# Optimization experiments

Hardware: AMD Instinct MI355X
Metric: run time of the kernel (lower is better)

The kernel has to match this reference:

```python
import jax, jax.numpy as jnp
import numpy as np

# Matcher thresholds from detectron2 RPN defaults
IOU_LO, IOU_HI = 0.3, 0.7            # anchor_matcher
OBJ_LO, OBJ_HI = 0.1, 0.3            # objectness_anchor_matcher (lower thresholds)
EPS = 1e-12


def _pairwise_iou(gt, anc):
    # gt: [G,4], anc: [A,4] (x1,y1,x2,y2) -> [G,A]
    area_g = (gt[:, 2] - gt[:, 0]) * (gt[:, 3] - gt[:, 1])
    area_a = (anc[:, 2] - anc[:, 0]) * (anc[:, 3] - anc[:, 1])
    lt = jnp.maximum(gt[:, None, :2], anc[None, :, :2])
    rb = jnp.minimum(gt[:, None, 2:], anc[None, :, 2:])
    wh = jnp.clip(rb - lt, 0.0)
    inter = wh[..., 0] * wh[..., 1]
    union = area_g[:, None] + area_a[None, :] - inter
    return jnp.where(inter > 0, inter / union, 0.0)


def _match(iou, lo, hi):
    # detectron2 Matcher with labels [0,-1,1] and allow_low_quality_matches=True
    vals = iou.max(axis=0)                      # [A]
    idxs = jnp.argmax(iou, axis=0)              # [A]
    labels = jnp.where(vals >= hi, 1, jnp.where(vals >= lo, -1, 0)).astype(jnp.int32)
    highest_per_gt = iou.max(axis=1)            # [G]
    low_quality = (iou == highest_per_gt[:, None]).any(axis=0)  # [A]
    labels = jnp.where(low_quality, 1, labels)
    return idxs, labels


def _get_deltas_linear(anc, tgt):
    # Box2BoxTransformLinear(normalize_by_size=True).get_deltas
    cx = 0.5 * (anc[:, 0] + anc[:, 2])
    cy = 0.5 * (anc[:, 1] + anc[:, 3])
    w = anc[:, 2] - anc[:, 0]
    h = anc[:, 3] - anc[:, 1]
    # order (l, t, r, b)
    deltas = jnp.stack([cx - tgt[:, 0], cy - tgt[:, 1], tgt[:, 2] - cx, tgt[:, 3] - cy], axis=-1)
    return deltas / jnp.stack([w, h, w, h], axis=-1)


def _label_one_image(gt_i, anchors):
    iou = _pairwise_iou(gt_i, anchors)                     # [G,A]
    m_idx, gt_labels = _match(iou, IOU_LO, IOU_HI)
    o_idx, obj_labels = _match(iou, OBJ_LO, OBJ_HI)
    matched_gt_boxes = gt_i[m_idx]                         # [A,4]
    # deltas reordered [:, [0,2,1,3]] -> (left, right, top, bottom)
    d = _get_deltas_linear(anchors, gt_i[o_idx])[:, jnp.array([0, 2, 1, 3])]
    in_box = (d >= 0).all(axis=-1)
    d = jnp.where(in_box[:, None], d, 0.0)
    lr, tb = d[:, 0:2], d[:, 2:4]
    prod = (lr.min(-1) / (lr.max(-1) + EPS)) * (tb.min(-1) / (tb.max(-1) + EPS))
    centerness = jnp.where(prod > 0, jnp.sqrt(jnp.where(prod > 0, prod, 1.0)), 0.0)
    centerness = jnp.where(obj_labels == 0, 0.0, centerness)
    return gt_labels, matched_gt_boxes, obj_labels, centerness


def setup_inputs() -> dict:
    key = jax.random.key(0)
    k1, k2, k3, k4 = jax.random.split(key, 4)
    A, B, G = 200000, 8, 32
    img_wh = jnp.array([1333.0, 800.0], dtype=jnp.float32)
    # anchors: random centers, sizes in [8, 264]
    a_ctr = jax.random.uniform(k1, (A, 2), dtype=jnp.float32) * img_wh
    a_wh = jax.random.uniform(k2, (A, 2), dtype=jnp.float32) * 256.0 + 8.0
    anchors = jnp.concatenate([a_ctr - 0.5 * a_wh, a_ctr + 0.5 * a_wh], axis=-1)
    # gt boxes: [B,G,4], sizes in [16, 416]
    g_ctr = jax.random.uniform(k3, (B, G, 2), dtype=jnp.float32) * img_wh
    g_wh = jax.random.uniform(k4, (B, G, 2), dtype=jnp.float32) * 400.0 + 16.0
    gt_boxes = jnp.concatenate([g_ctr - 0.5 * g_wh, g_ctr + 0.5 * g_wh], axis=-1)
    return {"gt_boxes": gt_boxes, "anchors": anchors}


def reference(gt_boxes, anchors):
    # gt_boxes: [B,G,4]; anchors: [A,4]
    gt_labels, matched_gt_boxes, obj_labels, centerness = jax.vmap(
        lambda g: _label_one_image(g, anchors)
    )(gt_boxes)
    return gt_labels, matched_gt_boxes, obj_labels, centerness
```

## Files before the change

kernel.cpp:

```cpp
#include <hip/hip_runtime.h>

#define G 32
#define APT 4
#define CHUNK (256 * APT)
#define SROW 68

__device__ __forceinline__ float iou_pre(float sum_area,
                                         float g0, float g1, float g2, float g3,
                                         float a0, float a1, float a2, float a3) {
#pragma clang fp contract(off)
    float ltx = fmaxf(g0, a0), lty = fmaxf(g1, a1);
    float rbx = fminf(g2, a2), rby = fminf(g3, a3);
    float wx = fmaxf(rbx - ltx, 0.0f), wy = fmaxf(rby - lty, 0.0f);
    float inter = wx * wy;
    float uni = sum_area - inter;
    return inter * __builtin_amdgcn_rcpf(uni);
}

__device__ __forceinline__ float centerness_fn(float4 an, float4 tb) {
#pragma clang fp contract(off)
    float cx = 0.5f * (an.x + an.z), cy = 0.5f * (an.y + an.w);
    float rw = __builtin_amdgcn_rcpf(an.z - an.x);
    float rh = __builtin_amdgcn_rcpf(an.w - an.y);
    float d0 = (cx - tb.x) * rw;
    float d1 = (tb.z - cx) * rw;
    float d2 = (cy - tb.y) * rh;
    float d3 = (tb.w - cy) * rh;
    bool inb = (d0 >= 0.0f) && (d1 >= 0.0f) && (d2 >= 0.0f) && (d3 >= 0.0f);
    if (!inb) { d0 = d1 = d2 = d3 = 0.0f; }
    float prod = (fminf(d0, d1) * __builtin_amdgcn_rcpf(fmaxf(d0, d1) + 1e-12f)) *
                 (fminf(d2, d3) * __builtin_amdgcn_rcpf(fmaxf(d2, d3) + 1e-12f));
    return prod > 0.0f ? sqrtf(prod) : 0.0f;
}

__global__ __launch_bounds__(256) void k1_main(const float* __restrict__ gt,
                                               const float* __restrict__ anchors,
                                               float* __restrict__ out,
                                               float* __restrict__ blockmax,
                                               float* __restrict__ hi,
                                               int A, int B) {
#pragma clang fp contract(off)
    __shared__ float4 s_gt[G];
    __shared__ float s_lm[G * SROW];
    const int c = blockIdx.x, b = blockIdx.y, t = threadIdx.x;
    if (t < G) s_gt[t] = ((const float4*)gt)[b * G + t];

    float4 an[APT];
    float aa[APT], best[APT];
    int bidx[APT];
    bool valid[APT];
    const int abase = c * CHUNK + t;
#pragma unroll
    for (int k = 0; k < APT; ++k) {
        int a = abase + k * 256;
        valid[k] = (a < A);
        int ac = valid[k] ? a : (A - 1);
        an[k] = ((const float4*)anchors)[ac];
        aa[k] = (an[k].z - an[k].x) * (an[k].w - an[k].y);
        best[k] = -1.0f;
        bidx[k] = 0;
    }

    const float4* __restrict__ gtb = ((const float4*)gt) + b * G;

#pragma unroll 4
    for (int g = 0; g < G; ++g) {
        const float4 gb = gtb[g];
        const float ag = (gb.z - gb.x) * (gb.w - gb.y);
        float v[APT];
#pragma unroll
        for (int k = 0; k < APT; ++k) {
            v[k] = iou_pre(ag + aa[k], gb.x, gb.y, gb.z, gb.w,
                           an[k].x, an[k].y, an[k].z, an[k].w);
            if (v[k] > best[k]) { best[k] = v[k]; bidx[k] = g; }
        }
        float lm = fmaxf(fmaxf(v[0], v[1]), fmaxf(v[2], v[3]));
        lm = fmaxf(lm, __shfl_xor(lm, 1, 64));
        lm = fmaxf(lm, __shfl_xor(lm, 2, 64));
        if ((t & 3) == 0) s_lm[g * SROW + (t >> 2)] = lm;
    }
    __syncthreads();

    {
        const int g = t >> 3, j = t & 7;
        const float4* p = (const float4*)&s_lm[g * SROW + j * 8];
        float4 q0 = p[0], q1 = p[1];
        float m = fmaxf(fmaxf(fmaxf(q0.x, q0.y), fmaxf(q0.z, q0.w)),
                        fmaxf(fmaxf(q1.x, q1.y), fmaxf(q1.z, q1.w)));
        m = fmaxf(m, __shfl_down(m, 4, 8));
        m = fmaxf(m, __shfl_down(m, 2, 8));
        m = fmaxf(m, __shfl_down(m, 1, 8));
        if (j == 0) {
            blockmax[(c * B + b) * G + g] = m;
            atomicMax((int*)&hi[b * G + g], (int)__float_as_int(m));
        }
    }

    const size_t BA = (size_t)B * (size_t)A;
    const size_t bA = (size_t)b * (size_t)A;
#pragma unroll
    for (int k = 0; k < APT; ++k) {
        if (!valid[k]) continue;
        const size_t o = bA + (size_t)(abase + k * 256);
        int gl = (best[k] >= 0.7f) ? 1 : ((best[k] >= 0.3f) ? -1 : 0);
        int ol = (best[k] >= 0.3f) ? 1 : ((best[k] >= 0.1f) ? -1 : 0);
        const float4 tb = s_gt[bidx[k]];
        float cen = centerness_fn(an[k], tb);
        if (ol == 0) cen = 0.0f;
        out[o] = (float)gl;
        ((float4*)(out + BA))[o] = tb;
        out[5 * BA + o] = (float)ol;
        out[6 * BA + o] = cen;
    }
}

__global__ __launch_bounds__(256) void k3_patch(const float* __restrict__ gt,
                                                const float* __restrict__ anchors,
                                                const float* __restrict__ blockmax,
                                                const float* __restrict__ hi,
                                                float* __restrict__ out,
                                                int A, int B) {
#pragma clang fp contract(off)
    __shared__ float4 s_gt[G];
    __shared__ float s_hi[G];
    __shared__ unsigned s_mask;
    const int c = blockIdx.x, b = blockIdx.y, t = threadIdx.x;
    bool fl = false;
    if (t < G) {
        float h = hi[b * G + t];
        s_hi[t] = h;
        s_gt[t] = ((const float4*)gt)[b * G + t];
        fl = (blockmax[(c * B + b) * G + t] == h);
    }
    unsigned long long m = __ballot(fl);
    if (t == 0) s_mask = (unsigned)(m & 0xffffffffull);
    __syncthreads();
    const unsigned mask0 = s_mask;
    if (mask0 == 0) return;

    const size_t BA = (size_t)B * (size_t)A;
    const size_t bA = (size_t)b * (size_t)A;
    const int abase = c * CHUNK + t;

#pragma unroll
    for (int k = 0; k < APT; ++k) {
        const int a = abase + k * 256;
        if (a >= A) continue;
        const float4 an = ((const float4*)anchors)[a];
        const float aa = (an.z - an.x) * (an.w - an.y);
        bool lq = false;
        unsigned mask = mask0;
        while (mask) {
            const int g = __ffs(mask) - 1;
            mask &= mask - 1;
            const float4 gb = s_gt[g];
            const float ag = (gb.z - gb.x) * (gb.w - gb.y);
            const float v = iou_pre(ag + aa, gb.x, gb.y, gb.z, gb.w,
                                    an.x, an.y, an.z, an.w);
            lq |= (v == s_hi[g]);
        }
        if (lq) {
            const size_t o = bA + (size_t)a;
            const float4 tb = ((const float4*)(out + BA))[o];
            const float cen = centerness_fn(an, tb);
            out[o] = 1.0f;
            out[5 * BA + o] = 1.0f;
            out[6 * BA + o] = cen;
        }
    }
}

extern "C" void kernel_launch(void* const* d_in, const int* in_sizes, int n_in,
                              void* d_out, int out_size, void* d_ws, size_t ws_size,
                              hipStream_t stream) {
    const float* gt = (const float*)d_in[0];
    const float* anchors = (const float*)d_in[1];
    float* out = (float*)d_out;

    const int B = in_sizes[0] / (G * 4);
    const int A = in_sizes[1] / 4;
    const int C = (A + CHUNK - 1) / CHUNK;

    float* hi = (float*)d_ws;
    float* blockmax = (float*)((char*)d_ws + 1024);

    k1_main<<<dim3(C, B), 256, 0, stream>>>(gt, anchors, out, blockmax, hi, A, B);
    k3_patch<<<dim3(C, B), 256, 0, stream>>>(gt, anchors, blockmax, hi, out, A, B);
}
```

Baseline: 111.6 us.

## Fuse main and low-quality patch kernels via cooperative grid sync

Merges the main labeling kernel and the low-quality-match patch kernel into one cooperative launch separated by a grid-wide barrier. Per-block maxima are kept in shared memory, and anchors and matched boxes stay in registers, so the second pass needs no global reloads. This removes one kernel launch and the blockmax round-trip. It adds host occupancy queries, needs the whole grid to be co-resident, and falls back to the two-kernel path otherwise.

```diff
diff --git a/kernel.cpp b/kernel.cpp
--- a/kernel.cpp
+++ b/kernel.cpp
@@ -1,4 +1,7 @@
 #include <hip/hip_runtime.h>
+#include <hip/hip_cooperative_groups.h>
+
+namespace cg = cooperative_groups;
 
 #define G 32
 #define APT 4
@@ -31,6 +34,128 @@
     float prod = (fminf(d0, d1) * __builtin_amdgcn_rcpf(fmaxf(d0, d1) + 1e-12f)) *
                  (fminf(d2, d3) * __builtin_amdgcn_rcpf(fmaxf(d2, d3) + 1e-12f));
     return prod > 0.0f ? sqrtf(prod) : 0.0f;
+}
+
+__global__ __launch_bounds__(256) void k_fused(const float* __restrict__ gt,
+                                               const float* __restrict__ anchors,
+                                               float* __restrict__ out,
+                                               float* __restrict__ hi,
+                                               int A, int B) {
+#pragma clang fp contract(off)
+    __shared__ float4 s_gt[G];
+    __shared__ float s_lm[G * SROW];
+    __shared__ float s_bm[G];
+    __shared__ float s_hi[G];
+    __shared__ unsigned s_mask;
+    const int c = blockIdx.x, b = blockIdx.y, t = threadIdx.x;
+    if (t < G) s_gt[t] = ((const float4*)gt)[b * G + t];
+
+    float4 an[APT];
+    float aa[APT], best[APT];
+    int bidx[APT];
+    bool valid[APT];
+    const int abase = c * CHUNK + t;
+#pragma unroll
+    for (int k = 0; k < APT; ++k) {
+        int a = abase + k * 256;
+        valid[k] = (a < A);
+        int ac = valid[k] ? a : (A - 1);
+        an[k] = ((const float4*)anchors)[ac];
+        aa[k] = (an[k].z - an[k].x) * (an[k].w - an[k].y);
+        best[k] = -1.0f;
+        bidx[k] = 0;
+    }
+
+    const float4* __restrict__ gtb = ((const float4*)gt) + b * G;
+
+#pragma unroll 4
+    for (int g = 0; g < G; ++g) {
+        const float4 gb = gtb[g];
+        const float ag = (gb.z - gb.x) * (gb.w - gb.y);
+        float v[APT];
+#pragma unroll
+        for (int k = 0; k < APT; ++k) {
+            v[k] = iou_pre(ag + aa[k], gb.x, gb.y, gb.z, gb.w,
+                           an[k].x, an[k].y, an[k].z, an[k].w);
+            if (v[k] > best[k]) { best[k] = v[k]; bidx[k] = g; }
+        }
+        float lm = fmaxf(fmaxf(v[0], v[1]), fmaxf(v[2], v[3]));
+        lm = fmaxf(lm, __shfl_xor(lm, 1, 64));
+        lm = fmaxf(lm, __shfl_xor(lm, 2, 64));
+        if ((t & 3) == 0) s_lm[g * SROW + (t >> 2)] = lm;
+    }
+    __syncthreads();
+
+    {
+        const int g = t >> 3, j = t & 7;
+        const float4* p = (const float4*)&s_lm[g * SROW + j * 8];
+        float4 q0 = p[0], q1 = p[1];
+        float m = fmaxf(fmaxf(fmaxf(q0.x, q0.y), fmaxf(q0.z, q0.w)),
+                        fmaxf(fmaxf(q1.x, q1.y), fmaxf(q1.z, q1.w)));
+        m = fmaxf(m, __shfl_down(m, 4, 8));
+        m = fmaxf(m, __shfl_down(m, 2, 8));
+        m = fmaxf(m, __shfl_down(m, 1, 8));
+        if (j == 0) {
+            s_bm[g] = m;
+            atomicMax((int*)&hi[b * G + g], (int)__float_as_int(m));
+        }
+    }
+
+    const size_t BA = (size_t)B * (size_t)A;
+    const size_t bA = (size_t)b * (size_t)A;
+#pragma unroll
+    for (int k = 0; k < APT; ++k) {
+        if (!valid[k]) continue;
+        const size_t o = bA + (size_t)(abase + k * 256);
+        int gl = (best[k] >= 0.7f) ? 1 : ((best[k] >= 0.3f) ? -1 : 0);
+        int ol = (best[k] >= 0.3f) ? 1 : ((best[k] >= 0.1f) ? -1 : 0);
+        const float4 tb = s_gt[bidx[k]];
+        float cen = centerness_fn(an[k], tb);
+        if (ol == 0) cen = 0.0f;
+        out[o] = (float)gl;
+        ((float4*)(out + BA))[o] = tb;
+        out[5 * BA + o] = (float)ol;
+        out[6 * BA + o] = cen;
+    }
+
+    cg::this_grid().sync();
+
+    bool fl = false;
+    if (t < G) {
+        int hbits = atomicOr((int*)&hi[b * G + t], 0);
+        float h = __int_as_float(hbits);
+        s_hi[t] = h;
+        fl = (s_bm[t] == h);
+    }
+    unsigned long long mm = __ballot(fl);
+    if (t == 0) s_mask = (unsigned)(mm & 0xffffffffull);
+    __syncthreads();
+    const unsigned mask0 = s_mask;
+    if (mask0 == 0) return;
+
+#pragma unroll
+    for (int k = 0; k < APT; ++k) {
+        if (!valid[k]) continue;
+        bool lq = false;
+        unsigned mask = mask0;
+        while (mask) {
+            const int g = __ffs(mask) - 1;
+            mask &= mask - 1;
+            const float4 gb = s_gt[g];
+            const float ag = (gb.z - gb.x) * (gb.w - gb.y);
+            const float v = iou_pre(ag + aa[k], gb.x, gb.y, gb.z, gb.w,
+                                    an[k].x, an[k].y, an[k].z, an[k].w);
+            lq |= (v == s_hi[g]);
+        }
+        if (lq) {
+            const size_t o = bA + (size_t)(abase + k * 256);
+            const float4 tb = s_gt[bidx[k]];
+            const float cen = centerness_fn(an[k], tb);
+            out[o] = 1.0f;
+            out[5 * BA + o] = 1.0f;
+            out[6 * BA + o] = cen;
+        }
+    }
 }
 
 __global__ __launch_bounds__(256) void k1_main(const float* __restrict__ gt,
@@ -184,6 +309,19 @@
     float* hi = (float*)d_ws;
     float* blockmax = (float*)((char*)d_ws + 1024);
 
-    k1_main<<<dim3(C, B), 256, 0, stream>>>(gt, anchors, out, blockmax, hi, A, B);
-    k3_patch<<<dim3(C, B), 256, 0, stream>>>(gt, anchors, blockmax, hi, out, A, B);
-}
+    int dev = 0, ncu = 0, maxb = 0;
+    (void)hipGetDevice(&dev);
+    (void)hipDeviceGetAttribute(&ncu, hipDeviceAttributeMultiprocessorCount, dev);
+    (void)hipOccupancyMaxActiveBlocksPerMultiprocessor(
+        &maxb, reinterpret_cast<const void*>(&k_fused), 256, 0);
+
+    if ((long long)maxb * (long long)ncu >= (long long)C * (long long)B) {
+        void* args[] = {(void*)&gt, (void*)&anchors, (void*)&out,
+                        (void*)&hi, (void*)&A, (void*)&B};
+        (void)hipLaunchCooperativeKernel(reinterpret_cast<const void*>(&k_fused),
+                                         dim3(C, B), dim3(256), args, 0, stream);
+    } else {
+        k1_main<<<dim3(C, B), 256, 0, stream>>>(gt, anchors, out, blockmax, hi, A, B);
+        k3_patch<<<dim3(C, B), 256, 0, stream>>>(gt, anchors, blockmax, hi, out, A, B);
+    }
+}
```

New measurement: 111.2 us. About the same (-0.4%).
